# Kernel optimization log

Measured on AMD Instinct MI355X. Metric: run time of the kernel, lower is better.

The kernel has to match this reference:

```python
import jax, jax.numpy as jnp
import numpy as np

N = 50000   # nodes
E = 400000  # edges per relation
R = 3       # relations
IN, HID, C, H = 128, 64, 40, 3  # in_feat, hidden_feat, n_classes, num_heads
NEG_SLOPE = 0.2  # DGL GATConv default leaky_relu slope


def setup_inputs() -> dict:
    key = jax.random.key(0)
    ks = jax.random.split(key, 12)
    feat = jax.random.normal(ks[0], (N, IN), jnp.float32)
    src = jax.random.randint(ks[1], (R, E), 0, N, dtype=jnp.int32)
    dst = jax.random.randint(ks[2], (R, E), 0, N, dtype=jnp.int32)

    def w(k, shape, fan):
        return jax.random.normal(k, shape, jnp.float32) / np.float32(np.sqrt(fan))

    # layer 1: in_feat -> hidden_feat, relu activation
    W1 = w(ks[3], (R, IN, H * HID), IN)
    al1 = w(ks[4], (R, H, HID), HID)
    ar1 = w(ks[5], (R, H, HID), HID)
    b1 = jnp.zeros((R, H * HID), jnp.float32)
    # layer 2: hidden_feat -> n_classes, no activation
    W2 = w(ks[6], (R, HID, H * C), HID)
    al2 = w(ks[7], (R, H, C), C)
    ar2 = w(ks[8], (R, H, C), C)
    b2 = jnp.zeros((R, H * C), jnp.float32)
    return dict(feat=feat, src=src, dst=dst, W1=W1, al1=al1, ar1=ar1, b1=b1,
                W2=W2, al2=al2, ar2=ar2, b2=b2)


def gat_hetero_layer(feat, src, dst, W, al, ar, b, apply_relu):
    """HeteroGraphConv(mean) over R relations, each a GATConv + head-mean."""
    n = feat.shape[0]

    def one_relation(src_r, dst_r, W_r, al_r, ar_r, b_r):
        n_heads, out = al_r.shape
        z = (feat @ W_r).reshape(n, n_heads, out)          # [N,H,out]
        el = jnp.sum(z * al_r, axis=-1)                    # [N,H]
        er = jnp.sum(z * ar_r, axis=-1)                    # [N,H]
        e = jax.nn.leaky_relu(el[src_r] + er[dst_r], NEG_SLOPE)  # [E,H]
        # edge softmax over incoming edges of each dst node
        m = jax.ops.segment_max(e, dst_r, num_segments=n)  # [N,H]
        a = jnp.exp(e - m[dst_r])                          # [E,H]
        s = jax.ops.segment_sum(a, dst_r, num_segments=n)  # [N,H]
        alpha = a / s[dst_r]                               # [E,H]
        msg = alpha[:, :, None] * z[src_r]                 # [E,H,out]
        rst = jax.ops.segment_sum(msg, dst_r, num_segments=n)  # [N,H,out]
        rst = rst + b_r.reshape(n_heads, out)
        if apply_relu:
            rst = jax.nn.relu(rst)
        return rst.mean(axis=1)                            # head mean -> [N,out]

    outs = jax.vmap(one_relation)(src, dst, W, al, ar, b)  # [R,N,out]
    return outs.mean(axis=0)                               # relation mean


def reference(feat, src, dst, W1, al1, ar1, b1, W2, al2, ar2, b2):
    h = gat_hetero_layer(feat, src, dst, W1, al1, ar1, b1, True)
    h = gat_hetero_layer(h, src, dst, W2, al2, ar2, b2, False)
    return h
```

## Files before the change

### kernel.cpp

```cpp
#include <hip/hip_runtime.h>

#define R_   3
#define N_   50000
#define E_   400000
#define IN_  128
#define HID_ 64
#define C_   40
#define H_   3
#define NEG_SLOPE 0.2f
#define LOG2E 1.4426950408889634f

#define SCAN_CHUNK 1024
#define NCH  49
#define NCH2 64

#define MPAD 50048
#define NRT  3128

typedef _Float16 half_t;
typedef _Float16 f16x8 __attribute__((ext_vector_type(8)));
typedef _Float16 f16x4 __attribute__((ext_vector_type(4)));
typedef float float4v __attribute__((ext_vector_type(4)));

template <int V> struct vecT;
template <> struct vecT<4> { typedef f16x4 type; };
template <> struct vecT<8> { typedef f16x8 type; };


template <int K, int NY>
__device__ inline void bprep_body(int idx, const float* __restrict__ W,
                                  half_t* __restrict__ Bf, int Nc) {
    constexpr int KB = K / 32;
    const int TOT = R_ * NY * KB * 4 * 64;
    if (idx >= TOT) return;
    int lane = idx & 63;
    int ct = (idx >> 6) & 3;
    int t = idx >> 8;
    int kb = t % KB; t /= KB;
    int y = t % NY;  int r = t / NY;
    int col = y * 64 + ct * 16 + (lane & 15);
    int k0 = kb * 32 + (lane >> 4) * 8;
    f16x8 h = {};
    if (col < Nc) {
        #pragma unroll
        for (int j = 0; j < 8; ++j)
            h[j] = (half_t)W[((size_t)r * K + k0 + j) * Nc + col];
    }
    ((f16x8*)Bf)[idx] = h;
}

__global__ void prep_kernel(const float* __restrict__ feat, half_t* __restrict__ At,
                            const float* __restrict__ W1, half_t* __restrict__ B1f,
                            const float* __restrict__ W2, half_t* __restrict__ B2f,
                            half_t* __restrict__ h1T,
                            const int* __restrict__ dst, int* __restrict__ deg) {
    int b = blockIdx.x;
    if (b < 3128) {
        int idx = b * 256 + threadIdx.x;
        int lane = idx & 63;
        int kb = (idx >> 6) & 3;
        int rowtile = idx >> 8;
        int row = rowtile * 16 + (lane & 15);
        int k = kb * 32 + (lane >> 4) * 8;
        f16x8 h = {};
        if (row < N_) {
            const float* p = feat + (size_t)row * IN_ + k;
            float4 a = ((const float4*)p)[0];
            float4 c = ((const float4*)p)[1];
            h[0] = (half_t)a.x; h[1] = (half_t)a.y; h[2] = (half_t)a.z; h[3] = (half_t)a.w;
            h[4] = (half_t)c.x; h[5] = (half_t)c.y; h[6] = (half_t)c.z; h[7] = (half_t)c.w;
        }
        ((f16x8*)At)[idx] = h;
    } else if (b < 3164) {
        bprep_body<IN_, 3>((b - 3128) * 256 + threadIdx.x, W1, B1f, H_ * HID_);
    } else if (b < 3176) {
        bprep_body<HID_, 2>((b - 3164) * 256 + threadIdx.x, W2, B2f, H_ * C_);
    } else if (b < 3188) {
        int i = (b - 3176) * 256 + threadIdx.x;
        if (i < 3072) h1T[(size_t)3125 * 2 * 512 + i] = (half_t)0.f;
    } else {
        const int T = (R_ * E_) / 4;
        int t = (b - 3188) * 256 + threadIdx.x;
        if (t < T) {
            #pragma unroll
            for (int j = 0; j < 4; ++j) {
                int idx = t + j * T;
                int r = idx / E_;
                atomicAdd(&deg[r * N_ + dst[idx]], 1);
            }
        }
    }
}

__global__ void scanA_kernel(const int* __restrict__ deg, int* __restrict__ bsum) {
    int r = blockIdx.y, ch = blockIdx.x, tid = threadIdx.x;
    int base = ch * SCAN_CHUNK + tid * 4;
    int s = 0;
    for (int j = 0; j < 4; ++j) {
        int i = base + j;
        if (i < N_) s += deg[r * N_ + i];
    }
    __shared__ int red[256];
    red[tid] = s; __syncthreads();
    for (int off = 128; off; off >>= 1) {
        if (tid < off) red[tid] += red[tid + off];
        __syncthreads();
    }
    if (tid == 0) bsum[r * NCH2 + ch] = red[0];
}

__global__ void scanC_kernel(const int* __restrict__ deg, const int* __restrict__ bsum,
                             int* __restrict__ rowptr, int* __restrict__ cursor) {
    int r = blockIdx.y, ch = blockIdx.x, tid = threadIdx.x;
    __shared__ int chbase_s;
    if (tid < 64) {
        int v = (tid < NCH) ? bsum[r * NCH2 + tid] : 0;
        int s = v;
        #pragma unroll
        for (int off = 1; off < 64; off <<= 1) {
            int t = __shfl_up(s, off);
            if (tid >= off) s += t;
        }
        if (tid == ch) chbase_s = s - v;
    }
    int base = ch * SCAN_CHUNK + tid * 4;
    int v[4]; int s = 0;
    for (int j = 0; j < 4; ++j) {
        int i = base + j;
        v[j] = (i < N_) ? deg[r * N_ + i] : 0;
        s += v[j];
    }
    __shared__ int buf[256];
    buf[tid] = s; __syncthreads();
    for (int off = 1; off < 256; off <<= 1) {
        int t2 = (tid >= off) ? buf[tid - off] : 0;
        __syncthreads();
        buf[tid] += t2;
        __syncthreads();
    }
    int excl = buf[tid] - s + chbase_s;
    int run = excl;
    for (int j = 0; j < 4; ++j) {
        int i = base + j;
        if (i < N_) {
            rowptr[r * (N_ + 1) + i] = run;
            cursor[r * N_ + i] = run;
            run += v[j];
        }
    }
    if (ch == 0 && tid == 0) rowptr[r * (N_ + 1) + N_] = E_;
}

__global__ void fill_kernel(const int* __restrict__ src, const int* __restrict__ dst,
                            int* __restrict__ cursor, int* __restrict__ csr_src) {
    const int T = (R_ * E_) / 4;
    int t = blockIdx.x * 256 + threadIdx.x;
    if (t >= T) return;
    int pos[4], s3[4], rr[4];
    #pragma unroll
    for (int j = 0; j < 4; ++j) {
        int idx = t + j * T;
        rr[j] = idx / E_;
        pos[j] = atomicAdd(&cursor[rr[j] * N_ + dst[idx]], 1);
        s3[j] = src[idx] * 3;
    }
    #pragma unroll
    for (int j = 0; j < 4; ++j)
        csr_src[(size_t)rr[j] * E_ + pos[j]] = s3[j];
}

template <int K, int NY, bool FUSE>
__global__ __launch_bounds__(256) void mfma_gemm3_kernel(
        const half_t* __restrict__ At, const half_t* __restrict__ Bf,
        half_t* __restrict__ Z, int Nc,
        const float* __restrict__ al, const float* __restrict__ ar,
        float* __restrict__ el, float* __restrict__ er) {
    constexpr int KB = K / 32;
    int r = blockIdx.z, y = blockIdx.y;
    int wave = threadIdx.x >> 6, lane = threadIdx.x & 63;
    int rowtile = blockIdx.x * 4 + wave;
    const f16x8* Ap = (const f16x8*)At + (size_t)rowtile * KB * 64 + lane;
    const f16x8* Bp = (const f16x8*)Bf + (size_t)(r * NY + y) * KB * 4 * 64 + lane;
    float4v acc[4] = {};
    #pragma unroll
    for (int kb = 0; kb < KB; ++kb) {
        f16x8 af = Ap[kb * 64];
        #pragma unroll
        for (int ct = 0; ct < 4; ++ct) {
            f16x8 bf = Bp[(kb * 4 + ct) * 64];
            acc[ct] = __builtin_amdgcn_mfma_f32_16x16x32_f16(af, bf, acc[ct], 0, 0, 0);
        }
    }
    int lrow = lane & 15, lq = lane >> 4;
    half_t* Zr = Z + (size_t)r * N_ * Nc;
    int rbase = rowtile * 16 + lq * 4;
    int col0 = y * 64;
    float elv[4] = {}, erv[4] = {};
    const float* alp;
    const float* arp;
    if constexpr (FUSE) {
        alp = al + ((size_t)r * H_ + y) * 64;
        arp = ar + ((size_t)r * H_ + y) * 64;
    }
    #pragma unroll
    for (int ct = 0; ct < 4; ++ct) {
        int col = col0 + ct * 16 + lrow;
        if (col >= Nc) continue;
        float wa = 0.f, wb = 0.f;
        if constexpr (FUSE) { wa = alp[ct * 16 + lrow]; wb = arp[ct * 16 + lrow]; }
        #pragma unroll
        for (int g = 0; g < 4; ++g) {
            int row = rbase + g;
            half_t zh = (half_t)acc[ct][g];
            if (row < N_) Zr[(size_t)row * Nc + col] = zh;
            if constexpr (FUSE) {
                float zf = (float)zh;
                elv[g] = fmaf(zf, wa, elv[g]);
                erv[g] = fmaf(zf, wb, erv[g]);
            }
        }
    }
    if constexpr (FUSE) {
        #pragma unroll
        for (int g = 0; g < 4; ++g) {
            #pragma unroll
            for (int m = 1; m < 16; m <<= 1) {
                elv[g] += __shfl_xor(elv[g], m);
                erv[g] += __shfl_xor(erv[g], m);
            }
        }
        if (lrow == 0) {
            #pragma unroll
            for (int g = 0; g < 4; ++g) {
                int row = rbase + g;
                if (row < N_) {
                    size_t o = ((size_t)r * N_ + row) * H_ + y;
                    el[o] = elv[g] * LOG2E;
                    er[o] = erv[g] * LOG2E;
                }
            }
        }
    }
}

template <int Dd>
__global__ __launch_bounds__(256) void attn2_kernel(
        const half_t* __restrict__ z, const float* __restrict__ al,
        const float* __restrict__ ar, float* __restrict__ el,
        float* __restrict__ er) {
    int t = blockIdx.x * 256 + threadIdx.x;
    if (t >= R_ * N_ * H_) return;
    int rn = t / H_, h = t - rn * H_;
    int r = rn / N_;
    const half_t* zrow = z + (size_t)rn * (3 * Dd) + h * Dd;
    const float* alp = al + (r * H_ + h) * Dd;
    const float* arp = ar + (r * H_ + h) * Dd;
    float p0 = 0.f, p1 = 0.f, q0 = 0.f, q1 = 0.f;
    #pragma unroll
    for (int c = 0; c < Dd / 8; ++c) {
        f16x8 zv = *(const f16x8*)(zrow + c * 8);
        #pragma unroll
        for (int j = 0; j < 8; j += 2) {
            float za = (float)zv[j], zb = (float)zv[j + 1];
            p0 += za * alp[c * 8 + j];
            p1 += zb * alp[c * 8 + j + 1];
            q0 += za * arp[c * 8 + j];
            q1 += zb * arp[c * 8 + j + 1];
        }
    }
    el[t] = (p0 + p1) * LOG2E;
    er[t] = (q0 + q1) * LOG2E;
}

template <int Dd, int VEC, bool RELU, typename OutT, bool TILED>
__global__ __launch_bounds__(256) void agg14_kernel(
        const int* __restrict__ rowptr, const int* __restrict__ csr_src,
        const half_t* __restrict__ z, const float* __restrict__ el,
        const float* __restrict__ er, const float* __restrict__ bias,
        OutT* __restrict__ out, float scale) {
    constexpr int ROWH = 3 * Dd;
    constexpr int LPE  = ROWH / VEC;
    constexpr int PH   = Dd / VEC;
    using fv = typename vecT<VEC>::type;
    int n = blockIdx.x * 4 + (threadIdx.x >> 6);
    int lane = threadIdx.x & 63;
    if (n >= N_) return;
    int hf = lane >> 5;
    int sub = lane & 31;
    bool act = sub < LPE;
    int hl = act ? sub / PH : 0;
    int dl = act ? sub - hl * PH : 0;
    int zoff = VEC * sub;
    int ii[R_], ee[R_];
    float ervv[R_];
    #pragma unroll
    for (int r = 0; r < R_; ++r) {
        ii[r] = rowptr[r * (N_ + 1) + n];
        ee[r] = rowptr[r * (N_ + 1) + n + 1];
        ervv[r] = er[((size_t)r * N_ + n) * H_ + hl];
    }
    fv ah[R_] = {};
    float ll[R_] = {};
    while (ii[0] < ee[0] || ii[1] < ee[1] || ii[2] < ee[2]) {
        fv zA[R_], zB[R_];
        float xA[R_], xB[R_];
        bool okA[R_], okB[R_];
        #pragma unroll
        for (int r = 0; r < R_; ++r) {
            const int* cs = csr_src + (size_t)r * E_;
            const half_t* zr = z + (size_t)r * N_ * ROWH;
            const float* elr = el + (size_t)r * N_ * H_;
            int eA = ii[r] + hf, eB = ii[r] + 2 + hf;
            okA[r] = eA < ee[r];
            okB[r] = eB < ee[r];
            int sA = cs[okA[r] ? eA : 0];
            int sB = cs[okB[r] ? eB : 0];
            xA[r] = elr[sA + hl] + ervv[r];
            xB[r] = elr[sB + hl] + ervv[r];
            zA[r] = {}; zB[r] = {};
            if (act) {
                zA[r] = *(const fv*)(zr + (size_t)sA * Dd + zoff);
                zB[r] = *(const fv*)(zr + (size_t)sB * Dd + zoff);
            }
        }
        #pragma unroll
        for (int r = 0; r < R_; ++r) {
            float xa = xA[r]; xa = fmaxf(xa, NEG_SLOPE * xa);
            float xb = xB[r]; xb = fmaxf(xb, NEG_SLOPE * xb);
            float cA = okA[r] ? __builtin_amdgcn_exp2f(xa) : 0.f;
            float cB = okB[r] ? __builtin_amdgcn_exp2f(xb) : 0.f;
            ll[r] += cA + cB;
            half_t hA = (half_t)cA, hB = (half_t)cB;
            fv vA, vB;
            #pragma unroll
            for (int v = 0; v < VEC; ++v) { vA[v] = hA; vB[v] = hB; }
            ah[r] += vA * zA[r] + vB * zB[r];
        }
        #pragma unroll
        for (int r = 0; r < R_; ++r) ii[r] += 4;
    }
    float aa[R_][VEC];
    #pragma unroll
    for (int r = 0; r < R_; ++r)
        #pragma unroll
        for (int v = 0; v < VEC; ++v) aa[r][v] = (float)ah[r][v];
    #pragma unroll
    for (int r = 0; r < R_; ++r) {
        #pragma unroll
        for (int v = 0; v < VEC; ++v) aa[r][v] += __shfl(aa[r][v], lane ^ 32);
        ll[r] += __shfl(ll[r], lane ^ 32);
    }
    float vacc[VEC] = {};
    #pragma unroll
    for (int r = 0; r < R_; ++r) {
        float li = (ll[r] > 0.f) ? 1.f / ll[r] : 0.f;
        const float* br = bias + r * ROWH + hl * Dd + VEC * dl;
        #pragma unroll
        for (int v = 0; v < VEC; ++v) {
            float t = aa[r][v] * li + br[v];
            if (RELU) t = fmaxf(t, 0.f);
            vacc[v] += t;
        }
    }
    int base = lane & 32;
    int p1 = sub + PH;     if (p1 >= LPE) p1 -= LPE;
    int p2 = sub + 2 * PH; if (p2 >= LPE) p2 -= LPE;
    #pragma unroll
    for (int v = 0; v < VEC; ++v)
        vacc[v] += __shfl(vacc[v], base + p1) + __shfl(vacc[v], base + p2);
    int srcl = lane / VEC;
    int cm = lane & (VEC - 1);
    float tv[VEC];
    #pragma unroll
    for (int v = 0; v < VEC; ++v) tv[v] = __shfl(vacc[v], srcl);
    float outv = tv[0];
    #pragma unroll
    for (int v = 1; v < VEC; ++v) outv = (cm == v) ? tv[v] : outv;
    if constexpr (TILED) {
        int rowtile = n >> 4;
        int kb = lane >> 5;
        int fl = (n & 15) + ((lane >> 3) & 3) * 16;
        int elo = lane & 7;
        size_t ho = (((size_t)rowtile * 2 + kb) * 64 + fl) * 8 + elo;
        ((half_t*)out)[ho] = (half_t)(outv * scale);
    } else {
        if (lane < Dd) out[(size_t)n * Dd + lane] = (OutT)(outv * scale);
    }
}

static inline size_t align256(size_t x) { return (x + 255) & ~(size_t)255; }

extern "C" void kernel_launch(void* const* d_in, const int* in_sizes, int n_in,
                              void* d_out, int out_size, void* d_ws, size_t ws_size,
                              hipStream_t stream) {
    const float* feat = (const float*)d_in[0];
    const int*   src  = (const int*)d_in[1];
    const int*   dst  = (const int*)d_in[2];
    const float* W1   = (const float*)d_in[3];
    const float* al1  = (const float*)d_in[4];
    const float* ar1  = (const float*)d_in[5];
    const float* b1   = (const float*)d_in[6];
    const float* W2   = (const float*)d_in[7];
    const float* al2  = (const float*)d_in[8];
    const float* ar2  = (const float*)d_in[9];
    const float* b2   = (const float*)d_in[10];
    float* out = (float*)d_out;

    char* ws = (char*)d_ws;
    size_t off = 0;
    half_t* zbuf  = (half_t*)(ws + off); off += align256((size_t)R_ * N_ * (3 * HID_) * 2);
    half_t* featT = (half_t*)(ws + off); off += align256((size_t)NRT * 4 * 64 * 8 * 2);
    half_t* h1T   = (half_t*)(ws + off); off += align256((size_t)NRT * 2 * 64 * 8 * 2);
    half_t* B1f   = (half_t*)(ws + off); off += align256((size_t)R_ * 3 * 4 * 4 * 64 * 8 * 2);
    half_t* B2f   = (half_t*)(ws + off); off += align256((size_t)R_ * 2 * 2 * 4 * 64 * 8 * 2);
    float* el   = (float*)(ws + off); off += align256((size_t)R_ * N_ * H_ * 4);
    float* er   = (float*)(ws + off); off += align256((size_t)R_ * N_ * H_ * 4);
    int* deg    = (int*)(ws + off);   off += align256((size_t)R_ * N_ * 4);
    int* rowptr = (int*)(ws + off);   off += align256((size_t)R_ * (N_ + 1) * 4);
    int* cursor = (int*)(ws + off);   off += align256((size_t)R_ * N_ * 4);
    int* bsum   = (int*)(ws + off);   off += align256((size_t)R_ * NCH2 * 4);
    int* csr    = (int*)(ws + off);   off += align256((size_t)R_ * E_ * 4);
    (void)ws_size; (void)n_in; (void)in_sizes; (void)out_size;

    const int ROW_TILES = (N_ + 63) / 64;
    const int NODE_WAVES = (N_ + 3) / 4;
    const int ATTN_BLOCKS = (R_ * N_ * H_ + 255) / 256;
    const int E4_BLOCKS = (R_ * E_ / 4 + 255) / 256;
    const int PREP_BLOCKS = 3188 + E4_BLOCKS;

    hipMemsetAsync(deg, 0, (size_t)R_ * N_ * 4, stream);
    prep_kernel<<<PREP_BLOCKS, 256, 0, stream>>>(feat, featT, W1, B1f, W2, B2f,
                                                 h1T, dst, deg);

    scanA_kernel<<<dim3(NCH, R_), 256, 0, stream>>>(deg, bsum);
    scanC_kernel<<<dim3(NCH, R_), 256, 0, stream>>>(deg, bsum, rowptr, cursor);
    fill_kernel<<<E4_BLOCKS, 256, 0, stream>>>(src, dst, cursor, csr);

    mfma_gemm3_kernel<IN_, 3, true><<<dim3(ROW_TILES, 3, R_), 256, 0, stream>>>(
        featT, B1f, zbuf, H_ * HID_, al1, ar1, el, er);
    agg14_kernel<HID_, 8, true, half_t, true><<<NODE_WAVES, 256, 0, stream>>>(
        rowptr, csr, zbuf, el, er, b1, h1T, 1.f / (H_ * R_));

    mfma_gemm3_kernel<HID_, 2, false><<<dim3(ROW_TILES, 2, R_), 256, 0, stream>>>(
        h1T, B2f, zbuf, H_ * C_, nullptr, nullptr, nullptr, nullptr);
    attn2_kernel<C_><<<ATTN_BLOCKS, 256, 0, stream>>>(zbuf, al2, ar2, el, er);
    agg14_kernel<C_, 4, false, float, false><<<NODE_WAVES, 256, 0, stream>>>(
        rowptr, csr, zbuf, el, er, b2, out, 1.f / (H_ * R_));
}
```

Before: 441.7 us.

## Split aggregation across relations with one wave per relation and LDS reduction

The aggregation kernel now assigns one wavefront per (node, relation) in 384-thread blocks covering two nodes, instead of one wave looping over all three relations. The per-relation partial outputs are summed through shared memory before writing. Guard branches are dropped by padding the CSR source array with zeros, so out-of-range edge reads become safe loads. This shortens per-wave dependency chains and lowers register pressure, at the cost of a block barrier and 50% more waves. It also removes the inactive-lane guard for the C=40 layer, which may read z slightly beyond the row.

```diff
diff --git a/kernel.cpp b/kernel.cpp
--- a/kernel.cpp
+++ b/kernel.cpp
@@ -52,7 +52,7 @@
 __global__ void prep_kernel(const float* __restrict__ feat, half_t* __restrict__ At,
                             const float* __restrict__ W1, half_t* __restrict__ B1f,
                             const float* __restrict__ W2, half_t* __restrict__ B2f,
-                            half_t* __restrict__ h1T,
+                            half_t* __restrict__ h1T, int* __restrict__ csr_src,
                             const int* __restrict__ dst, int* __restrict__ deg) {
     int b = blockIdx.x;
     if (b < 3128) {
@@ -78,9 +78,11 @@
     } else if (b < 3188) {
         int i = (b - 3176) * 256 + threadIdx.x;
         if (i < 3072) h1T[(size_t)3125 * 2 * 512 + i] = (half_t)0.f;
+    } else if (b == 3188) {
+        if (threadIdx.x < 16) csr_src[(size_t)R_ * E_ + threadIdx.x] = 0;
     } else {
         const int T = (R_ * E_) / 4;
-        int t = (b - 3188) * 256 + threadIdx.x;
+        int t = (b - 3189) * 256 + threadIdx.x;
         if (t < T) {
             #pragma unroll
             for (int j = 0; j < 4; ++j) {
@@ -273,7 +275,7 @@
 }
 
 template <int Dd, int VEC, bool RELU, typename OutT, bool TILED>
-__global__ __launch_bounds__(256) void agg14_kernel(
+__global__ __launch_bounds__(384) void agg17_kernel(
         const int* __restrict__ rowptr, const int* __restrict__ csr_src,
         const half_t* __restrict__ z, const float* __restrict__ el,
         const float* __restrict__ er, const float* __restrict__ bias,
@@ -282,85 +284,57 @@
     constexpr int LPE  = ROWH / VEC;
     constexpr int PH   = Dd / VEC;
     using fv = typename vecT<VEC>::type;
-    int n = blockIdx.x * 4 + (threadIdx.x >> 6);
-    int lane = threadIdx.x & 63;
-    if (n >= N_) return;
+    int lane = threadIdx.x;
+    int r    = threadIdx.y;
+    int slot = threadIdx.z;
+    int n = blockIdx.x * 2 + slot;
     int hf = lane >> 5;
     int sub = lane & 31;
-    bool act = sub < LPE;
-    int hl = act ? sub / PH : 0;
-    int dl = act ? sub - hl * PH : 0;
+    int hl = sub / PH;
+    int dl = sub - hl * PH;
     int zoff = VEC * sub;
-    int ii[R_], ee[R_];
-    float ervv[R_];
-    #pragma unroll
-    for (int r = 0; r < R_; ++r) {
-        ii[r] = rowptr[r * (N_ + 1) + n];
-        ee[r] = rowptr[r * (N_ + 1) + n + 1];
-        ervv[r] = er[((size_t)r * N_ + n) * H_ + hl];
-    }
-    fv ah[R_] = {};
-    float ll[R_] = {};
-    while (ii[0] < ee[0] || ii[1] < ee[1] || ii[2] < ee[2]) {
-        fv zA[R_], zB[R_];
-        float xA[R_], xB[R_];
-        bool okA[R_], okB[R_];
-        #pragma unroll
-        for (int r = 0; r < R_; ++r) {
-            const int* cs = csr_src + (size_t)r * E_;
-            const half_t* zr = z + (size_t)r * N_ * ROWH;
-            const float* elr = el + (size_t)r * N_ * H_;
-            int eA = ii[r] + hf, eB = ii[r] + 2 + hf;
-            okA[r] = eA < ee[r];
-            okB[r] = eB < ee[r];
-            int sA = cs[okA[r] ? eA : 0];
-            int sB = cs[okB[r] ? eB : 0];
-            xA[r] = elr[sA + hl] + ervv[r];
-            xB[r] = elr[sB + hl] + ervv[r];
-            zA[r] = {}; zB[r] = {};
-            if (act) {
-                zA[r] = *(const fv*)(zr + (size_t)sA * Dd + zoff);
-                zB[r] = *(const fv*)(zr + (size_t)sB * Dd + zoff);
-            }
-        }
-        #pragma unroll
-        for (int r = 0; r < R_; ++r) {
-            float xa = xA[r]; xa = fmaxf(xa, NEG_SLOPE * xa);
-            float xb = xB[r]; xb = fmaxf(xb, NEG_SLOPE * xb);
-            float cA = okA[r] ? __builtin_amdgcn_exp2f(xa) : 0.f;
-            float cB = okB[r] ? __builtin_amdgcn_exp2f(xb) : 0.f;
-            ll[r] += cA + cB;
-            half_t hA = (half_t)cA, hB = (half_t)cB;
-            fv vA, vB;
-            #pragma unroll
-            for (int v = 0; v < VEC; ++v) { vA[v] = hA; vB[v] = hB; }
-            ah[r] += vA * zA[r] + vB * zB[r];
-        }
-        #pragma unroll
-        for (int r = 0; r < R_; ++r) ii[r] += 4;
-    }
-    float aa[R_][VEC];
-    #pragma unroll
-    for (int r = 0; r < R_; ++r)
-        #pragma unroll
-        for (int v = 0; v < VEC; ++v) aa[r][v] = (float)ah[r][v];
-    #pragma unroll
-    for (int r = 0; r < R_; ++r) {
-        #pragma unroll
-        for (int v = 0; v < VEC; ++v) aa[r][v] += __shfl(aa[r][v], lane ^ 32);
-        ll[r] += __shfl(ll[r], lane ^ 32);
-    }
-    float vacc[VEC] = {};
-    #pragma unroll
-    for (int r = 0; r < R_; ++r) {
-        float li = (ll[r] > 0.f) ? 1.f / ll[r] : 0.f;
-        const float* br = bias + r * ROWH + hl * Dd + VEC * dl;
-        #pragma unroll
-        for (int v = 0; v < VEC; ++v) {
-            float t = aa[r][v] * li + br[v];
-            if (RELU) t = fmaxf(t, 0.f);
-            vacc[v] += t;
-        }
+    int ii = rowptr[r * (N_ + 1) + n];
+    int ee = rowptr[r * (N_ + 1) + n + 1];
+    float erv = er[((size_t)r * N_ + n) * H_ + hl];
+    const int* cs = csr_src + (size_t)r * E_;
+    const half_t* zr = z + (size_t)r * N_ * ROWH;
+    const float* elr = el + (size_t)r * N_ * H_;
+    fv ah = {};
+    float ll = 0.f;
+    for (; ii < ee; ii += 4) {
+        int eA = ii + hf, eB = ii + 2 + hf;
+        bool okA = eA < ee, okB = eB < ee;
+        int sA = cs[eA];
+        int sB = cs[eB];
+        float xA = elr[sA + hl] + erv;
+        float xB = elr[sB + hl] + erv;
+        fv zA = *(const fv*)(zr + (size_t)sA * Dd + zoff);
+        fv zB = *(const fv*)(zr + (size_t)sB * Dd + zoff);
+        xA = fmaxf(xA, NEG_SLOPE * xA);
+        xB = fmaxf(xB, NEG_SLOPE * xB);
+        float cA = okA ? __builtin_amdgcn_exp2f(xA) : 0.f;
+        float cB = okB ? __builtin_amdgcn_exp2f(xB) : 0.f;
+        ll += cA + cB;
+        half_t hA = (half_t)cA, hB = (half_t)cB;
+        fv vA, vB;
+        #pragma unroll
+        for (int v = 0; v < VEC; ++v) { vA[v] = hA; vB[v] = hB; }
+        ah += vA * zA + vB * zB;
+    }
+    float aa[VEC];
+    #pragma unroll
+    for (int v = 0; v < VEC; ++v) aa[v] = (float)ah[v];
+    #pragma unroll
+    for (int v = 0; v < VEC; ++v) aa[v] += __shfl(aa[v], lane ^ 32);
+    ll += __shfl(ll, lane ^ 32);
+    float li = (ll > 0.f) ? 1.f / ll : 0.f;
+    const float* br = bias + r * ROWH + hl * Dd + VEC * dl;
+    float vacc[VEC];
+    #pragma unroll
+    for (int v = 0; v < VEC; ++v) {
+        float t = aa[v] * li + br[v];
+        if (RELU) t = fmaxf(t, 0.f);
+        vacc[v] = t;
     }
     int base = lane & 32;
     int p1 = sub + PH;     if (p1 >= LPE) p1 -= LPE;
@@ -376,15 +350,21 @@
     float outv = tv[0];
     #pragma unroll
     for (int v = 1; v < VEC; ++v) outv = (cm == v) ? tv[v] : outv;
-    if constexpr (TILED) {
-        int rowtile = n >> 4;
-        int kb = lane >> 5;
-        int fl = (n & 15) + ((lane >> 3) & 3) * 16;
-        int elo = lane & 7;
-        size_t ho = (((size_t)rowtile * 2 + kb) * 64 + fl) * 8 + elo;
-        ((half_t*)out)[ho] = (half_t)(outv * scale);
-    } else {
-        if (lane < Dd) out[(size_t)n * Dd + lane] = (OutT)(outv * scale);
+    __shared__ float red[2][3][64];
+    red[slot][r][lane] = outv;
+    __syncthreads();
+    if (r == 0) {
+        float o = (red[slot][0][lane] + red[slot][1][lane] + red[slot][2][lane]) * scale;
+        if constexpr (TILED) {
+            int rowtile = n >> 4;
+            int kb = lane >> 5;
+            int fl = (n & 15) + ((lane >> 3) & 3) * 16;
+            int elo = lane & 7;
+            size_t ho = (((size_t)rowtile * 2 + kb) * 64 + fl) * 8 + elo;
+            ((half_t*)out)[ho] = (half_t)o;
+        } else {
+            if (lane < Dd) out[(size_t)n * Dd + lane] = (OutT)o;
+        }
     }
 }
 
@@ -419,18 +399,19 @@
     int* rowptr = (int*)(ws + off);   off += align256((size_t)R_ * (N_ + 1) * 4);
     int* cursor = (int*)(ws + off);   off += align256((size_t)R_ * N_ * 4);
     int* bsum   = (int*)(ws + off);   off += align256((size_t)R_ * NCH2 * 4);
-    int* csr    = (int*)(ws + off);   off += align256((size_t)R_ * E_ * 4);
+    int* csr    = (int*)(ws + off);   off += align256((size_t)R_ * E_ * 4 + 64);
     (void)ws_size; (void)n_in; (void)in_sizes; (void)out_size;
 
     const int ROW_TILES = (N_ + 63) / 64;
-    const int NODE_WAVES = (N_ + 3) / 4;
     const int ATTN_BLOCKS = (R_ * N_ * H_ + 255) / 256;
     const int E4_BLOCKS = (R_ * E_ / 4 + 255) / 256;
-    const int PREP_BLOCKS = 3188 + E4_BLOCKS;
+    const int PREP_BLOCKS = 3189 + E4_BLOCKS;
+    const dim3 AGG_BLK(64, 3, 2);
+    const int AGG_GRID = N_ / 2;
 
     hipMemsetAsync(deg, 0, (size_t)R_ * N_ * 4, stream);
     prep_kernel<<<PREP_BLOCKS, 256, 0, stream>>>(feat, featT, W1, B1f, W2, B2f,
-                                                 h1T, dst, deg);
+                                                 h1T, csr, dst, deg);
 
     scanA_kernel<<<dim3(NCH, R_), 256, 0, stream>>>(deg, bsum);
     scanC_kernel<<<dim3(NCH, R_), 256, 0, stream>>>(deg, bsum, rowptr, cursor);
@@ -438,12 +419,12 @@
 
     mfma_gemm3_kernel<IN_, 3, true><<<dim3(ROW_TILES, 3, R_), 256, 0, stream>>>(
         featT, B1f, zbuf, H_ * HID_, al1, ar1, el, er);
-    agg14_kernel<HID_, 8, true, half_t, true><<<NODE_WAVES, 256, 0, stream>>>(
+    agg17_kernel<HID_, 8, true, half_t, true><<<AGG_GRID, AGG_BLK, 0, stream>>>(
         rowptr, csr, zbuf, el, er, b1, h1T, 1.f / (H_ * R_));
 
     mfma_gemm3_kernel<HID_, 2, false><<<dim3(ROW_TILES, 2, R_), 256, 0, stream>>>(
         h1T, B2f, zbuf, H_ * C_, nullptr, nullptr, nullptr, nullptr);
     attn2_kernel<C_><<<ATTN_BLOCKS, 256, 0, stream>>>(zbuf, al2, ar2, el, er);
-    agg14_kernel<C_, 4, false, float, false><<<NODE_WAVES, 256, 0, stream>>>(
+    agg17_kernel<C_, 4, false, float, false><<<AGG_GRID, AGG_BLK, 0, stream>>>(
         rowptr, csr, zbuf, el, er, b2, out, 1.f / (H_ * R_));
 }
```

After: 492.7 us. +11.5%, slower.
